# Performance work log

Measured on AMD Instinct MI355X. Metric: run time of the kernel, lower is better.

## Reference

```python
import jax, jax.numpy as jnp
import numpy as np

IN_FEATURES = 16384
OUT_FEATURES = 16384
NNZ = 1_000_000
BATCH = 256


def setup_inputs() -> dict:
    key = jax.random.key(0)
    k1, k2, k3 = jax.random.split(key, 3)
    x = jax.random.normal(k1, (IN_FEATURES, BATCH), dtype=jnp.float32)
    values = jax.random.normal(k2, (NNZ,), dtype=jnp.float32)
    indices = jax.random.randint(k3, (2, NNZ), 0, OUT_FEATURES, dtype=jnp.int64)
    bias = jnp.zeros((OUT_FEATURES, 1), dtype=jnp.float32)
    return {"x": x, "values": values, "indices": indices, "bias": bias}


def reference(x, values, indices, bias):
    # Sparse (COO) matmul: out[r, :] += values[k] * x[c, :] for each nnz (r, c).
    # Equivalent to torch.sparse.mm(W_coo.coalesce(), x) + bias since
    # coalesce() sums duplicate entries and segment_sum does the same.
    row = indices[0]  # [nnz] in [0, OUT_FEATURES)
    col = indices[1]  # [nnz] in [0, IN_FEATURES)
    gathered = values[:, None] * x[col]  # [nnz, B]
    out = jax.ops.segment_sum(gathered, row, num_segments=OUT_FEATURES)  # [out, B]
    return out + bias
```

## Files before the change

### kernel.cpp

```cpp
#include <hip/hip_runtime.h>

typedef unsigned int u32;
typedef unsigned short u16;
typedef unsigned long long u64;

constexpr int OUT_F = 16384;
constexpr int IN_F  = 16384;
constexpr int B_N   = 256;
constexpr int NG    = 512;
constexpr int GCAP  = 2368;
constexpr int BINB  = 4096;


__global__ __launch_bounds__(1024) void prep_k(
    const int* __restrict__ rows, const int* __restrict__ cols,
    const float* __restrict__ vals, const float* __restrict__ x,
    u16* __restrict__ xb, int* __restrict__ gcnt,
    uint2* __restrict__ gbuck, int nnz, int nbin, int n4) {
  const int tid = threadIdx.x;

  if ((int)blockIdx.x >= nbin) {
    const int i2 = blockIdx.x - nbin;
    for (int j = 0; j < 4; ++j) {
      int k4 = i2 * 4096 + j * 1024 + tid;
      if (k4 < n4) {
        float4 v = ((const float4*)x)[k4];
        u32 u0 = __float_as_uint(v.x), u1 = __float_as_uint(v.y),
            u2 = __float_as_uint(v.z), u3 = __float_as_uint(v.w);
        ushort4 r;
        r.x = (u16)((u0 + 0x7FFFu + ((u0 >> 16) & 1u)) >> 16);
        r.y = (u16)((u1 + 0x7FFFu + ((u1 >> 16) & 1u)) >> 16);
        r.z = (u16)((u2 + 0x7FFFu + ((u2 >> 16) & 1u)) >> 16);
        r.w = (u16)((u3 + 0x7FFFu + ((u3 >> 16) & 1u)) >> 16);
        ((ushort4*)xb)[k4] = r;
      }
    }
    return;
  }

  __shared__ int   hist[NG], lofs[NG], cur[NG], gbase[NG];
  __shared__ int   wsum[8];
  __shared__ uint2 stage[BINB];
  __shared__ int   tgt[BINB];

  const int base = blockIdx.x * BINB;
  const int nval = min(BINB, nnz - base);
  if (tid < NG) hist[tid] = 0;
  __syncthreads();

  int r[4]; u32 c[4]; float v[4]; bool ok[4];
#pragma unroll
  for (int i = 0; i < 4; ++i) {
    int k = base + i * 1024 + tid;
    ok[i] = k < nnz;
    if (ok[i]) {
      r[i] = __builtin_nontemporal_load(&rows[k]);
      c[i] = (u32)__builtin_nontemporal_load(&cols[k]);
      v[i] = __builtin_nontemporal_load(&vals[k]);
      atomicAdd(&hist[r[i] >> 5], 1);
    }
  }
  __syncthreads();

  const int lane = tid & 63;
  const int wv   = tid >> 6;
  int hv = 0, incl = 0;
  if (tid < NG) {
    hv = hist[tid];
    incl = hv;
#pragma unroll
    for (int d = 1; d < 64; d <<= 1) {
      int t = __shfl_up(incl, d, 64);
      if (lane >= d) incl += t;
    }
    if (lane == 63) wsum[wv] = incl;
  }
  __syncthreads();
  if (tid == 0) {
    int run = 0;
#pragma unroll
    for (int w = 0; w < NG / 64; ++w) { int t = wsum[w]; wsum[w] = run; run += t; }
  }
  __syncthreads();
  if (tid < NG) {
    int excl = incl - hv + wsum[wv];
    lofs[tid] = excl;
    cur[tid]  = excl;
    gbase[tid] = atomicAdd(&gcnt[tid], hv);
  }
  __syncthreads();

#pragma unroll
  for (int i = 0; i < 4; ++i) {
    if (ok[i]) {
      int g   = r[i] >> 5;
      int pos = atomicAdd(&cur[g], 1);
      stage[pos].x = (c[i] << 5) | (u32)(r[i] & 31);
      stage[pos].y = __float_as_uint(v[i]);
      int w = gbase[g] + (pos - lofs[g]);
      tgt[pos] = (w < GCAP) ? (g * GCAP + w) : -1;
    }
  }
  __syncthreads();

#pragma unroll
  for (int j = 0; j < 4; ++j) {
    int idx = j * 1024 + tid;
    if (idx < nval) {
      int t = tgt[idx];
      if (t >= 0) gbuck[t] = stage[idx];
    }
  }
}

__global__ __launch_bounds__(1024) void sortspmm_k(
    const int* __restrict__ gcnt, const uint2* __restrict__ gbuck,
    const u16* __restrict__ xb, const float* __restrict__ bias,
    float* __restrict__ out) {
  __shared__ int hist[2048];
  __shared__ int wsum[16];
  __shared__ u32 pk_lds[GCAP];
  __shared__ int rs[32], rc[32];
  const int tid = threadIdx.x;
  const int g   = blockIdx.x;
  int cnt = gcnt[g];
  if (cnt > GCAP) cnt = GCAP;
  const uint2* bk = gbuck + (size_t)g * GCAP;

#pragma unroll
  for (int i = 0; i < 2; ++i) hist[i * 1024 + tid] = 0;
  __syncthreads();

  uint2 e[3]; int bin[3]; bool ok[3];
#pragma unroll
  for (int i = 0; i < 3; ++i) {
    int k = i * 1024 + tid;
    ok[i] = k < cnt;
    if (ok[i]) {
      u64 q = __builtin_nontemporal_load((const u64*)&bk[k]);
      e[i].x = (u32)q; e[i].y = (u32)(q >> 32);
      bin[i] = (int)(((e[i].x & 31u) << 6) | (e[i].x >> 13));
      atomicAdd(&hist[bin[i]], 1);
    }
  }
  __syncthreads();

  const int lane = tid & 63;
  const int wv   = tid >> 6;
  int loc0 = hist[tid * 2], loc1 = hist[tid * 2 + 1];
  int s = loc0 + loc1;
  int incl = s;
#pragma unroll
  for (int d = 1; d < 64; d <<= 1) {
    int t = __shfl_up(incl, d, 64);
    if (lane >= d) incl += t;
  }
  if (lane == 63) wsum[wv] = incl;
  __syncthreads();
  if (tid == 0) {
    int run = 0;
#pragma unroll
    for (int w = 0; w < 16; ++w) { int t = wsum[w]; wsum[w] = run; run += t; }
  }
  __syncthreads();
  int excl = incl - s + wsum[wv];
  hist[tid * 2]     = excl;
  hist[tid * 2 + 1] = excl + loc0;
  __syncthreads();

  if (tid < 32) {
    int lo = hist[tid << 6];
    int hi = (tid == 31) ? cnt : hist[(tid + 1) << 6];
    rs[tid] = lo;
    rc[tid] = hi - lo;
  }
  __syncthreads();

#pragma unroll
  for (int i = 0; i < 3; ++i) {
    if (ok[i]) {
      int pos = atomicAdd(&hist[bin[i]], 1);
      u32 col = e[i].x >> 5;
      pk_lds[pos] = (col << 18) | (e[i].y >> 14);
    }
  }
  __syncthreads();

  const int wid = tid >> 6;
  const int r0g = g * 32;

  for (int rr = 0; rr < 2; ++rr) {
    const int fr   = wid * 2 + rr;
    const int st   = rs[fr];
    const int cntr = rc[fr];
    float a0 = 0.f, a1 = 0.f, a2 = 0.f, a3 = 0.f;
    for (int base = 0; base < cntr; base += 64) {
      const int m = min(64, cntr - base);
      u32 pk = 0;
      if (lane < m) pk = pk_lds[st + base + lane];
      int j = 0;
      for (; j + 8 <= m; j += 8) {
        u32 e0 = (u32)__builtin_amdgcn_readlane((int)pk, j);
        u32 e1 = (u32)__builtin_amdgcn_readlane((int)pk, j + 1);
        u32 e2 = (u32)__builtin_amdgcn_readlane((int)pk, j + 2);
        u32 e3 = (u32)__builtin_amdgcn_readlane((int)pk, j + 3);
        u32 e4 = (u32)__builtin_amdgcn_readlane((int)pk, j + 4);
        u32 e5 = (u32)__builtin_amdgcn_readlane((int)pk, j + 5);
        u32 e6 = (u32)__builtin_amdgcn_readlane((int)pk, j + 6);
        u32 e7 = (u32)__builtin_amdgcn_readlane((int)pk, j + 7);
        uint2 x0 = ((const uint2*)(xb + ((size_t)(e0 >> 18) << 8)))[lane];
        uint2 x1 = ((const uint2*)(xb + ((size_t)(e1 >> 18) << 8)))[lane];
        uint2 x2 = ((const uint2*)(xb + ((size_t)(e2 >> 18) << 8)))[lane];
        uint2 x3 = ((const uint2*)(xb + ((size_t)(e3 >> 18) << 8)))[lane];
        uint2 x4 = ((const uint2*)(xb + ((size_t)(e4 >> 18) << 8)))[lane];
        uint2 x5 = ((const uint2*)(xb + ((size_t)(e5 >> 18) << 8)))[lane];
        uint2 x6 = ((const uint2*)(xb + ((size_t)(e6 >> 18) << 8)))[lane];
        uint2 x7 = ((const uint2*)(xb + ((size_t)(e7 >> 18) << 8)))[lane];
        float v0 = __uint_as_float(e0 << 14), v1 = __uint_as_float(e1 << 14);
        float v2 = __uint_as_float(e2 << 14), v3 = __uint_as_float(e3 << 14);
        float v4 = __uint_as_float(e4 << 14), v5 = __uint_as_float(e5 << 14);
        float v6 = __uint_as_float(e6 << 14), v7 = __uint_as_float(e7 << 14);
        a0 = fmaf(v0, __uint_as_float(x0.x << 16), a0);
        a1 = fmaf(v0, __uint_as_float(x0.x & 0xFFFF0000u), a1);
        a2 = fmaf(v0, __uint_as_float(x0.y << 16), a2);
        a3 = fmaf(v0, __uint_as_float(x0.y & 0xFFFF0000u), a3);
        a0 = fmaf(v1, __uint_as_float(x1.x << 16), a0);
        a1 = fmaf(v1, __uint_as_float(x1.x & 0xFFFF0000u), a1);
        a2 = fmaf(v1, __uint_as_float(x1.y << 16), a2);
        a3 = fmaf(v1, __uint_as_float(x1.y & 0xFFFF0000u), a3);
        a0 = fmaf(v2, __uint_as_float(x2.x << 16), a0);
        a1 = fmaf(v2, __uint_as_float(x2.x & 0xFFFF0000u), a1);
        a2 = fmaf(v2, __uint_as_float(x2.y << 16), a2);
        a3 = fmaf(v2, __uint_as_float(x2.y & 0xFFFF0000u), a3);
        a0 = fmaf(v3, __uint_as_float(x3.x << 16), a0);
        a1 = fmaf(v3, __uint_as_float(x3.x & 0xFFFF0000u), a1);
        a2 = fmaf(v3, __uint_as_float(x3.y << 16), a2);
        a3 = fmaf(v3, __uint_as_float(x3.y & 0xFFFF0000u), a3);
        a0 = fmaf(v4, __uint_as_float(x4.x << 16), a0);
        a1 = fmaf(v4, __uint_as_float(x4.x & 0xFFFF0000u), a1);
        a2 = fmaf(v4, __uint_as_float(x4.y << 16), a2);
        a3 = fmaf(v4, __uint_as_float(x4.y & 0xFFFF0000u), a3);
        a0 = fmaf(v5, __uint_as_float(x5.x << 16), a0);
        a1 = fmaf(v5, __uint_as_float(x5.x & 0xFFFF0000u), a1);
        a2 = fmaf(v5, __uint_as_float(x5.y << 16), a2);
        a3 = fmaf(v5, __uint_as_float(x5.y & 0xFFFF0000u), a3);
        a0 = fmaf(v6, __uint_as_float(x6.x << 16), a0);
        a1 = fmaf(v6, __uint_as_float(x6.x & 0xFFFF0000u), a1);
        a2 = fmaf(v6, __uint_as_float(x6.y << 16), a2);
        a3 = fmaf(v6, __uint_as_float(x6.y & 0xFFFF0000u), a3);
        a0 = fmaf(v7, __uint_as_float(x7.x << 16), a0);
        a1 = fmaf(v7, __uint_as_float(x7.x & 0xFFFF0000u), a1);
        a2 = fmaf(v7, __uint_as_float(x7.y << 16), a2);
        a3 = fmaf(v7, __uint_as_float(x7.y & 0xFFFF0000u), a3);
      }
      for (; j < m; ++j) {
        u32 ee = (u32)__builtin_amdgcn_readlane((int)pk, j);
        float v = __uint_as_float(ee << 14);
        uint2 xx = ((const uint2*)(xb + ((size_t)(ee >> 18) << 8)))[lane];
        a0 = fmaf(v, __uint_as_float(xx.x << 16), a0);
        a1 = fmaf(v, __uint_as_float(xx.x & 0xFFFF0000u), a1);
        a2 = fmaf(v, __uint_as_float(xx.y << 16), a2);
        a3 = fmaf(v, __uint_as_float(xx.y & 0xFFFF0000u), a3);
      }
    }
    const int rout = r0g + fr;
    const float bv = bias[rout];
    u64 lo = ((u64)__float_as_uint(a1 + bv) << 32) | (u64)__float_as_uint(a0 + bv);
    u64 hi = ((u64)__float_as_uint(a3 + bv) << 32) | (u64)__float_as_uint(a2 + bv);
    u64* dst = (u64*)(out + (size_t)rout * B_N + lane * 4);
    __builtin_nontemporal_store(lo, dst);
    __builtin_nontemporal_store(hi, dst + 1);
  }
}


__global__ __launch_bounds__(256) void hist_k(const int* __restrict__ rows,
                                              int* __restrict__ counts, int nnz) {
  int k = blockIdx.x * 256 + threadIdx.x;
  if (k < nnz) atomicAdd(&counts[rows[k]], 1);
}

__global__ __launch_bounds__(1024) void scan_k(const int* __restrict__ counts,
                                               int* __restrict__ offsets,
                                               int* __restrict__ cursor) {
  __shared__ int part[1024];
  const int tid  = threadIdx.x;
  const int base = tid * 16;
  int loc[16];
  int s = 0;
#pragma unroll
  for (int i = 0; i < 16; ++i) { loc[i] = counts[base + i]; s += loc[i]; }
  part[tid] = s;
  __syncthreads();
  for (int off = 1; off < 1024; off <<= 1) {
    int v = (tid >= off) ? part[tid - off] : 0;
    __syncthreads();
    part[tid] += v;
    __syncthreads();
  }
  int run = (tid == 0) ? 0 : part[tid - 1];
#pragma unroll
  for (int i = 0; i < 16; ++i) {
    offsets[base + i] = run;
    cursor[base + i]  = run;
    run += loc[i];
  }
  if (tid == 1023) offsets[OUT_F] = run;
}

__global__ __launch_bounds__(256) void scatter_k(const int* __restrict__ rows,
                                                 const int* __restrict__ colsIn,
                                                 const float* __restrict__ vals,
                                                 int* __restrict__ cursor,
                                                 int* __restrict__ colsOut,
                                                 float* __restrict__ valsOut,
                                                 int nnz) {
  int k = blockIdx.x * 256 + threadIdx.x;
  if (k < nnz) {
    int r   = rows[k];
    int pos = atomicAdd(&cursor[r], 1);
    colsOut[pos] = colsIn[k];
    valsOut[pos] = vals[k];
  }
}

__global__ __launch_bounds__(256) void spmm_k(const int* __restrict__ offsets,
                                              const int* __restrict__ cols,
                                              const float* __restrict__ vals,
                                              const float* __restrict__ x,
                                              const float* __restrict__ bias,
                                              float* __restrict__ out) {
  __shared__ int   c_lds[256];
  __shared__ float v_lds[256];
  const int r = blockIdx.x;
  const int b = threadIdx.x;
  const int start = offsets[r];
  const int end   = offsets[r + 1];
  float acc = 0.f;
  for (int basei = start; basei < end; basei += 256) {
    const int n = min(256, end - basei);
    if (threadIdx.x < n) {
      c_lds[threadIdx.x] = cols[basei + threadIdx.x];
      v_lds[threadIdx.x] = vals[basei + threadIdx.x];
    }
    __syncthreads();
    for (int j = 0; j < n; ++j) {
      acc = fmaf(v_lds[j], x[(size_t)c_lds[j] * B_N + b], acc);
    }
    __syncthreads();
  }
  out[(size_t)r * B_N + b] = acc + bias[r];
}


__global__ __launch_bounds__(256) void initout_k(const float* __restrict__ bias,
                                                 float* __restrict__ out) {
  int i = blockIdx.x * 256 + threadIdx.x;
  out[i] = bias[i >> 8];
}

__global__ __launch_bounds__(256) void atomic_k(const int* __restrict__ rows,
                                                const int* __restrict__ colsIn,
                                                const float* __restrict__ vals,
                                                const float* __restrict__ x,
                                                float* __restrict__ out, int nnz) {
  int k = blockIdx.x;
  if (k < nnz) {
    int r = rows[k], c = colsIn[k];
    float v = vals[k];
    int b = threadIdx.x;
    atomicAdd(&out[(size_t)r * B_N + b], v * x[(size_t)c * B_N + b]);
  }
}

extern "C" void kernel_launch(void* const* d_in, const int* in_sizes, int n_in,
                              void* d_out, int out_size, void* d_ws, size_t ws_size,
                              hipStream_t stream) {
  const float* x      = (const float*)d_in[0];
  const float* values = (const float*)d_in[1];
  const int*   idx    = (const int*)d_in[2];
  const float* bias   = (const float*)d_in[3];
  float* out = (float*)d_out;

  const int nnz = in_sizes[2] / 2;
  const int* rows   = idx;
  const int* colsIn = idx + nnz;

  char* ws = (char*)d_ws;
  auto align256 = [](size_t v) { return (v + 255) & ~(size_t)255; };

  size_t t1_gcnt  = 0;
  size_t t1_gbuck = align256(t1_gcnt + (size_t)NG * 4);
  size_t t1_xb    = align256(t1_gbuck + (size_t)NG * GCAP * 8);
  size_t t1_need  = align256(t1_xb + (size_t)IN_F * B_N * 2);

  size_t t2_counts  = 0;
  size_t t2_offsets = align256(t2_counts + (size_t)OUT_F * 4);
  size_t t2_cursor  = align256(t2_offsets + ((size_t)OUT_F + 1) * 4);
  size_t t2_cols    = align256(t2_cursor + (size_t)OUT_F * 4);
  size_t t2_vals    = align256(t2_cols + (size_t)nnz * 4);
  size_t t2_need    = align256(t2_vals + (size_t)nnz * 4);

  if (ws_size >= t1_need) {
    int*   gcnt  = (int*)(ws + t1_gcnt);
    uint2* gbuck = (uint2*)(ws + t1_gbuck);
    u16*   xb    = (u16*)(ws + t1_xb);

    const int n4   = IN_F * B_N / 4;
    const int nbin = (nnz + BINB - 1) / BINB;
    const int nxc  = (n4 + 4095) / 4096;

    hipMemsetAsync(gcnt, 0, (size_t)NG * 4, stream);
    prep_k<<<nbin + nxc, 1024, 0, stream>>>(rows, colsIn, values, x, xb, gcnt,
                                            gbuck, nnz, nbin, n4);
    sortspmm_k<<<NG, 1024, 0, stream>>>(gcnt, gbuck, xb, bias, out);
  } else if (ws_size >= t2_need) {
    int*   counts  = (int*)(ws + t2_counts);
    int*   offsets = (int*)(ws + t2_offsets);
    int*   cursor  = (int*)(ws + t2_cursor);
    int*   colsB   = (int*)(ws + t2_cols);
    float* valsB   = (float*)(ws + t2_vals);

    const int nblk = (nnz + 255) / 256;
    hipMemsetAsync(counts, 0, (size_t)OUT_F * 4, stream);
    hist_k<<<nblk, 256, 0, stream>>>(rows, counts, nnz);
    scan_k<<<1, 1024, 0, stream>>>(counts, offsets, cursor);
    scatter_k<<<nblk, 256, 0, stream>>>(rows, colsIn, values, cursor, colsB, valsB, nnz);
    spmm_k<<<OUT_F, 256, 0, stream>>>(offsets, colsB, valsB, x, bias, out);
  } else {
    initout_k<<<(out_size + 255) / 256, 256, 0, stream>>>(bias, out);
    atomic_k<<<nnz, 256, 0, stream>>>(rows, colsIn, values, x, out, nnz);
  }
}
```

Baseline: 68.24 us.

## Fuse memset, prep and sort-spmm into one cooperative kernel with grid syncs

Replaces the memset plus two kernel launches with a single cooperative kernel of 512 blocks. Each block zeroes its group count, then blocks either bin nonzeros or convert x to bf16, a grid sync follows, and then every block does the per-group sort and gather. The aim is to remove launch gaps and inter-kernel drain between stages, at the cost of grid-wide barriers, 1024-thread blocks that must all be co-resident, and fewer blocks for the x conversion. The old multi-kernel path stays as a fallback if the cooperative launch fails.

```diff
diff --git a/kernel.cpp b/kernel.cpp
--- a/kernel.cpp
+++ b/kernel.cpp
@@ -1,4 +1,5 @@
 #include <hip/hip_runtime.h>
+#include <hip/hip_cooperative_groups.h>
 
 typedef unsigned int u32;
 typedef unsigned short u16;
@@ -11,186 +12,12 @@
 constexpr int GCAP  = 2368;
 constexpr int BINB  = 4096;
 
-
-__global__ __launch_bounds__(1024) void prep_k(
-    const int* __restrict__ rows, const int* __restrict__ cols,
-    const float* __restrict__ vals, const float* __restrict__ x,
-    u16* __restrict__ xb, int* __restrict__ gcnt,
-    uint2* __restrict__ gbuck, int nnz, int nbin, int n4) {
-  const int tid = threadIdx.x;
-
-  if ((int)blockIdx.x >= nbin) {
-    const int i2 = blockIdx.x - nbin;
-    for (int j = 0; j < 4; ++j) {
-      int k4 = i2 * 4096 + j * 1024 + tid;
-      if (k4 < n4) {
-        float4 v = ((const float4*)x)[k4];
-        u32 u0 = __float_as_uint(v.x), u1 = __float_as_uint(v.y),
-            u2 = __float_as_uint(v.z), u3 = __float_as_uint(v.w);
-        ushort4 r;
-        r.x = (u16)((u0 + 0x7FFFu + ((u0 >> 16) & 1u)) >> 16);
-        r.y = (u16)((u1 + 0x7FFFu + ((u1 >> 16) & 1u)) >> 16);
-        r.z = (u16)((u2 + 0x7FFFu + ((u2 >> 16) & 1u)) >> 16);
-        r.w = (u16)((u3 + 0x7FFFu + ((u3 >> 16) & 1u)) >> 16);
-        ((ushort4*)xb)[k4] = r;
-      }
-    }
-    return;
-  }
-
-  __shared__ int   hist[NG], lofs[NG], cur[NG], gbase[NG];
-  __shared__ int   wsum[8];
-  __shared__ uint2 stage[BINB];
-  __shared__ int   tgt[BINB];
-
-  const int base = blockIdx.x * BINB;
-  const int nval = min(BINB, nnz - base);
-  if (tid < NG) hist[tid] = 0;
-  __syncthreads();
-
-  int r[4]; u32 c[4]; float v[4]; bool ok[4];
-#pragma unroll
-  for (int i = 0; i < 4; ++i) {
-    int k = base + i * 1024 + tid;
-    ok[i] = k < nnz;
-    if (ok[i]) {
-      r[i] = __builtin_nontemporal_load(&rows[k]);
-      c[i] = (u32)__builtin_nontemporal_load(&cols[k]);
-      v[i] = __builtin_nontemporal_load(&vals[k]);
-      atomicAdd(&hist[r[i] >> 5], 1);
-    }
-  }
-  __syncthreads();
-
-  const int lane = tid & 63;
-  const int wv   = tid >> 6;
-  int hv = 0, incl = 0;
-  if (tid < NG) {
-    hv = hist[tid];
-    incl = hv;
-#pragma unroll
-    for (int d = 1; d < 64; d <<= 1) {
-      int t = __shfl_up(incl, d, 64);
-      if (lane >= d) incl += t;
-    }
-    if (lane == 63) wsum[wv] = incl;
-  }
-  __syncthreads();
-  if (tid == 0) {
-    int run = 0;
-#pragma unroll
-    for (int w = 0; w < NG / 64; ++w) { int t = wsum[w]; wsum[w] = run; run += t; }
-  }
-  __syncthreads();
-  if (tid < NG) {
-    int excl = incl - hv + wsum[wv];
-    lofs[tid] = excl;
-    cur[tid]  = excl;
-    gbase[tid] = atomicAdd(&gcnt[tid], hv);
-  }
-  __syncthreads();
-
-#pragma unroll
-  for (int i = 0; i < 4; ++i) {
-    if (ok[i]) {
-      int g   = r[i] >> 5;
-      int pos = atomicAdd(&cur[g], 1);
-      stage[pos].x = (c[i] << 5) | (u32)(r[i] & 31);
-      stage[pos].y = __float_as_uint(v[i]);
-      int w = gbase[g] + (pos - lofs[g]);
-      tgt[pos] = (w < GCAP) ? (g * GCAP + w) : -1;
-    }
-  }
-  __syncthreads();
-
-#pragma unroll
-  for (int j = 0; j < 4; ++j) {
-    int idx = j * 1024 + tid;
-    if (idx < nval) {
-      int t = tgt[idx];
-      if (t >= 0) gbuck[t] = stage[idx];
-    }
-  }
-}
-
-__global__ __launch_bounds__(1024) void sortspmm_k(
-    const int* __restrict__ gcnt, const uint2* __restrict__ gbuck,
-    const u16* __restrict__ xb, const float* __restrict__ bias,
-    float* __restrict__ out) {
-  __shared__ int hist[2048];
-  __shared__ int wsum[16];
-  __shared__ u32 pk_lds[GCAP];
-  __shared__ int rs[32], rc[32];
-  const int tid = threadIdx.x;
-  const int g   = blockIdx.x;
-  int cnt = gcnt[g];
-  if (cnt > GCAP) cnt = GCAP;
-  const uint2* bk = gbuck + (size_t)g * GCAP;
-
-#pragma unroll
-  for (int i = 0; i < 2; ++i) hist[i * 1024 + tid] = 0;
-  __syncthreads();
-
-  uint2 e[3]; int bin[3]; bool ok[3];
-#pragma unroll
-  for (int i = 0; i < 3; ++i) {
-    int k = i * 1024 + tid;
-    ok[i] = k < cnt;
-    if (ok[i]) {
-      u64 q = __builtin_nontemporal_load((const u64*)&bk[k]);
-      e[i].x = (u32)q; e[i].y = (u32)(q >> 32);
-      bin[i] = (int)(((e[i].x & 31u) << 6) | (e[i].x >> 13));
-      atomicAdd(&hist[bin[i]], 1);
-    }
-  }
-  __syncthreads();
-
-  const int lane = tid & 63;
-  const int wv   = tid >> 6;
-  int loc0 = hist[tid * 2], loc1 = hist[tid * 2 + 1];
-  int s = loc0 + loc1;
-  int incl = s;
-#pragma unroll
-  for (int d = 1; d < 64; d <<= 1) {
-    int t = __shfl_up(incl, d, 64);
-    if (lane >= d) incl += t;
-  }
-  if (lane == 63) wsum[wv] = incl;
-  __syncthreads();
-  if (tid == 0) {
-    int run = 0;
-#pragma unroll
-    for (int w = 0; w < 16; ++w) { int t = wsum[w]; wsum[w] = run; run += t; }
-  }
-  __syncthreads();
-  int excl = incl - s + wsum[wv];
-  hist[tid * 2]     = excl;
-  hist[tid * 2 + 1] = excl + loc0;
-  __syncthreads();
-
-  if (tid < 32) {
-    int lo = hist[tid << 6];
-    int hi = (tid == 31) ? cnt : hist[(tid + 1) << 6];
-    rs[tid] = lo;
-    rc[tid] = hi - lo;
-  }
-  __syncthreads();
-
-#pragma unroll
-  for (int i = 0; i < 3; ++i) {
-    if (ok[i]) {
-      int pos = atomicAdd(&hist[bin[i]], 1);
-      u32 col = e[i].x >> 5;
-      pk_lds[pos] = (col << 18) | (e[i].y >> 14);
-    }
-  }
-  __syncthreads();
-
-  const int wid = tid >> 6;
+__device__ __forceinline__ void gather_rows(
+    const int* rs, const int* rc, const u32* pk_lds, const u16* xb,
+    const float* bias, float* out, int g, int lane, int wv, int rows_per_wave) {
   const int r0g = g * 32;
-
-  for (int rr = 0; rr < 2; ++rr) {
-    const int fr   = wid * 2 + rr;
+  for (int rr = 0; rr < rows_per_wave; ++rr) {
+    const int fr   = wv * rows_per_wave + rr;
     const int st   = rs[fr];
     const int cntr = rc[fr];
     float a0 = 0.f, a1 = 0.f, a2 = 0.f, a3 = 0.f;
@@ -273,6 +100,360 @@
   }
 }
 
+struct SmemA {
+  int histA[NG]; int lofs[NG]; int cur[NG]; int gbase[NG]; int wsumA[8];
+  uint2 stage[BINB]; int tgt[BINB];
+};
+struct SmemB {
+  int histB[2048]; int wsumB[16]; u32 pk_lds[GCAP]; int rs[32]; int rc[32];
+};
+union SmemU { SmemA a; SmemB b; };
+
+__global__ __launch_bounds__(1024) void mega_k(
+    const int* __restrict__ rows, const int* __restrict__ cols,
+    const float* __restrict__ vals, const float* __restrict__ x,
+    u16* __restrict__ xb, int* __restrict__ gcnt, uint2* __restrict__ gbuck,
+    const float* __restrict__ bias, float* __restrict__ out,
+    int nnz, int nbin, int n4) {
+  __shared__ SmemU sm;
+  cooperative_groups::grid_group grid = cooperative_groups::this_grid();
+  const int tid  = threadIdx.x;
+  const int b    = blockIdx.x;
+  const int lane = tid & 63;
+  const int wv   = tid >> 6;
+
+  if (tid == 0) gcnt[b] = 0;
+  grid.sync();
+
+  if (b < nbin) {
+    const int base = b * BINB;
+    const int nval = min(BINB, nnz - base);
+    if (tid < NG) sm.a.histA[tid] = 0;
+    __syncthreads();
+
+    int r[4]; u32 c[4]; float v[4]; bool ok[4];
+#pragma unroll
+    for (int i = 0; i < 4; ++i) {
+      int k = base + i * 1024 + tid;
+      ok[i] = k < nnz;
+      if (ok[i]) {
+        r[i] = __builtin_nontemporal_load(&rows[k]);
+        c[i] = (u32)__builtin_nontemporal_load(&cols[k]);
+        v[i] = __builtin_nontemporal_load(&vals[k]);
+        atomicAdd(&sm.a.histA[r[i] >> 5], 1);
+      }
+    }
+    __syncthreads();
+
+    int hv = 0, incl = 0;
+    if (tid < NG) {
+      hv = sm.a.histA[tid];
+      incl = hv;
+#pragma unroll
+      for (int d = 1; d < 64; d <<= 1) {
+        int t = __shfl_up(incl, d, 64);
+        if (lane >= d) incl += t;
+      }
+      if (lane == 63) sm.a.wsumA[wv] = incl;
+    }
+    __syncthreads();
+    if (tid == 0) {
+      int run = 0;
+#pragma unroll
+      for (int w = 0; w < NG / 64; ++w) { int t = sm.a.wsumA[w]; sm.a.wsumA[w] = run; run += t; }
+    }
+    __syncthreads();
+    if (tid < NG) {
+      int excl = incl - hv + sm.a.wsumA[wv];
+      sm.a.lofs[tid] = excl;
+      sm.a.cur[tid]  = excl;
+      sm.a.gbase[tid] = atomicAdd(&gcnt[tid], hv);
+    }
+    __syncthreads();
+
+#pragma unroll
+    for (int i = 0; i < 4; ++i) {
+      if (ok[i]) {
+        int g   = r[i] >> 5;
+        int pos = atomicAdd(&sm.a.cur[g], 1);
+        sm.a.stage[pos].x = (c[i] << 5) | (u32)(r[i] & 31);
+        sm.a.stage[pos].y = __float_as_uint(v[i]);
+        int w = sm.a.gbase[g] + (pos - sm.a.lofs[g]);
+        sm.a.tgt[pos] = (w < GCAP) ? (g * GCAP + w) : -1;
+      }
+    }
+    __syncthreads();
+
+#pragma unroll
+    for (int j = 0; j < 4; ++j) {
+      int idx = j * 1024 + tid;
+      if (idx < nval) {
+        int t = sm.a.tgt[idx];
+        if (t >= 0) gbuck[t] = sm.a.stage[idx];
+      }
+    }
+  } else {
+    const int nxc = NG - nbin;
+    const int per = (n4 + nxc - 1) / nxc;
+    const int s0  = (b - nbin) * per;
+    const int cnt4 = min(per, n4 - s0);
+    for (int j = tid; j < cnt4; j += 1024) {
+      float4 v = ((const float4*)x)[s0 + j];
+      u32 u0 = __float_as_uint(v.x), u1 = __float_as_uint(v.y),
+          u2 = __float_as_uint(v.z), u3 = __float_as_uint(v.w);
+      ushort4 rr;
+      rr.x = (u16)((u0 + 0x7FFFu + ((u0 >> 16) & 1u)) >> 16);
+      rr.y = (u16)((u1 + 0x7FFFu + ((u1 >> 16) & 1u)) >> 16);
+      rr.z = (u16)((u2 + 0x7FFFu + ((u2 >> 16) & 1u)) >> 16);
+      rr.w = (u16)((u3 + 0x7FFFu + ((u3 >> 16) & 1u)) >> 16);
+      ((ushort4*)xb)[s0 + j] = rr;
+    }
+  }
+  grid.sync();
+
+  const int g = b;
+  int cnt = gcnt[g];
+  if (cnt > GCAP) cnt = GCAP;
+  const uint2* bk = gbuck + (size_t)g * GCAP;
+
+#pragma unroll
+  for (int i = 0; i < 2; ++i) sm.b.histB[i * 1024 + tid] = 0;
+  __syncthreads();
+
+  uint2 e[3]; int bin[3]; bool ok[3];
+#pragma unroll
+  for (int i = 0; i < 3; ++i) {
+    int k = i * 1024 + tid;
+    ok[i] = k < cnt;
+    if (ok[i]) {
+      u64 q = __builtin_nontemporal_load((const u64*)&bk[k]);
+      e[i].x = (u32)q; e[i].y = (u32)(q >> 32);
+      bin[i] = (int)(((e[i].x & 31u) << 6) | (e[i].x >> 13));
+      atomicAdd(&sm.b.histB[bin[i]], 1);
+    }
+  }
+  __syncthreads();
+
+  int loc0 = sm.b.histB[tid * 2], loc1 = sm.b.histB[tid * 2 + 1];
+  int s = loc0 + loc1;
+  int incl = s;
+#pragma unroll
+  for (int d = 1; d < 64; d <<= 1) {
+    int t = __shfl_up(incl, d, 64);
+    if (lane >= d) incl += t;
+  }
+  if (lane == 63) sm.b.wsumB[wv] = incl;
+  __syncthreads();
+  if (tid == 0) {
+    int run = 0;
+#pragma unroll
+    for (int w = 0; w < 16; ++w) { int t = sm.b.wsumB[w]; sm.b.wsumB[w] = run; run += t; }
+  }
+  __syncthreads();
+  int excl = incl - s + sm.b.wsumB[wv];
+  sm.b.histB[tid * 2]     = excl;
+  sm.b.histB[tid * 2 + 1] = excl + loc0;
+  __syncthreads();
+
+  if (tid < 32) {
+    int lo = sm.b.histB[tid << 6];
+    int hi = (tid == 31) ? cnt : sm.b.histB[(tid + 1) << 6];
+    sm.b.rs[tid] = lo;
+    sm.b.rc[tid] = hi - lo;
+  }
+  __syncthreads();
+
+#pragma unroll
+  for (int i = 0; i < 3; ++i) {
+    if (ok[i]) {
+      int pos = atomicAdd(&sm.b.histB[bin[i]], 1);
+      u32 col = e[i].x >> 5;
+      sm.b.pk_lds[pos] = (col << 18) | (e[i].y >> 14);
+    }
+  }
+  __syncthreads();
+
+  gather_rows(sm.b.rs, sm.b.rc, sm.b.pk_lds, xb, bias, out, g, lane, wv, 2);
+}
+
+
+__global__ __launch_bounds__(1024) void prep_k(
+    const int* __restrict__ rows, const int* __restrict__ cols,
+    const float* __restrict__ vals, const float* __restrict__ x,
+    u16* __restrict__ xb, int* __restrict__ gcnt,
+    uint2* __restrict__ gbuck, int nnz, int nbin, int n4) {
+  const int tid = threadIdx.x;
+
+  if ((int)blockIdx.x >= nbin) {
+    const int i2 = blockIdx.x - nbin;
+    for (int j = 0; j < 4; ++j) {
+      int k4 = i2 * 4096 + j * 1024 + tid;
+      if (k4 < n4) {
+        float4 v = ((const float4*)x)[k4];
+        u32 u0 = __float_as_uint(v.x), u1 = __float_as_uint(v.y),
+            u2 = __float_as_uint(v.z), u3 = __float_as_uint(v.w);
+        ushort4 r;
+        r.x = (u16)((u0 + 0x7FFFu + ((u0 >> 16) & 1u)) >> 16);
+        r.y = (u16)((u1 + 0x7FFFu + ((u1 >> 16) & 1u)) >> 16);
+        r.z = (u16)((u2 + 0x7FFFu + ((u2 >> 16) & 1u)) >> 16);
+        r.w = (u16)((u3 + 0x7FFFu + ((u3 >> 16) & 1u)) >> 16);
+        ((ushort4*)xb)[k4] = r;
+      }
+    }
+    return;
+  }
+
+  __shared__ int   hist[NG], lofs[NG], cur[NG], gbase[NG];
+  __shared__ int   wsum[8];
+  __shared__ uint2 stage[BINB];
+  __shared__ int   tgt[BINB];
+
+  const int base = blockIdx.x * BINB;
+  const int nval = min(BINB, nnz - base);
+  if (tid < NG) hist[tid] = 0;
+  __syncthreads();
+
+  int r[4]; u32 c[4]; float v[4]; bool ok[4];
+#pragma unroll
+  for (int i = 0; i < 4; ++i) {
+    int k = base + i * 1024 + tid;
+    ok[i] = k < nnz;
+    if (ok[i]) {
+      r[i] = __builtin_nontemporal_load(&rows[k]);
+      c[i] = (u32)__builtin_nontemporal_load(&cols[k]);
+      v[i] = __builtin_nontemporal_load(&vals[k]);
+      atomicAdd(&hist[r[i] >> 5], 1);
+    }
+  }
+  __syncthreads();
+
+  const int lane = tid & 63;
+  const int wv   = tid >> 6;
+  int hv = 0, incl = 0;
+  if (tid < NG) {
+    hv = hist[tid];
+    incl = hv;
+#pragma unroll
+    for (int d = 1; d < 64; d <<= 1) {
+      int t = __shfl_up(incl, d, 64);
+      if (lane >= d) incl += t;
+    }
+    if (lane == 63) wsum[wv] = incl;
+  }
+  __syncthreads();
+  if (tid == 0) {
+    int run = 0;
+#pragma unroll
+    for (int w = 0; w < NG / 64; ++w) { int t = wsum[w]; wsum[w] = run; run += t; }
+  }
+  __syncthreads();
+  if (tid < NG) {
+    int excl = incl - hv + wsum[wv];
+    lofs[tid] = excl;
+    cur[tid]  = excl;
+    gbase[tid] = atomicAdd(&gcnt[tid], hv);
+  }
+  __syncthreads();
+
+#pragma unroll
+  for (int i = 0; i < 4; ++i) {
+    if (ok[i]) {
+      int g   = r[i] >> 5;
+      int pos = atomicAdd(&cur[g], 1);
+      stage[pos].x = (c[i] << 5) | (u32)(r[i] & 31);
+      stage[pos].y = __float_as_uint(v[i]);
+      int w = gbase[g] + (pos - lofs[g]);
+      tgt[pos] = (w < GCAP) ? (g * GCAP + w) : -1;
+    }
+  }
+  __syncthreads();
+
+#pragma unroll
+  for (int j = 0; j < 4; ++j) {
+    int idx = j * 1024 + tid;
+    if (idx < nval) {
+      int t = tgt[idx];
+      if (t >= 0) gbuck[t] = stage[idx];
+    }
+  }
+}
+
+__global__ __launch_bounds__(1024) void sortspmm_k(
+    const int* __restrict__ gcnt, const uint2* __restrict__ gbuck,
+    const u16* __restrict__ xb, const float* __restrict__ bias,
+    float* __restrict__ out) {
+  __shared__ int hist[2048];
+  __shared__ int wsum[16];
+  __shared__ u32 pk_lds[GCAP];
+  __shared__ int rs[32], rc[32];
+  const int tid = threadIdx.x;
+  const int g   = blockIdx.x;
+  int cnt = gcnt[g];
+  if (cnt > GCAP) cnt = GCAP;
+  const uint2* bk = gbuck + (size_t)g * GCAP;
+
+#pragma unroll
+  for (int i = 0; i < 2; ++i) hist[i * 1024 + tid] = 0;
+  __syncthreads();
+
+  uint2 e[3]; int bin[3]; bool ok[3];
+#pragma unroll
+  for (int i = 0; i < 3; ++i) {
+    int k = i * 1024 + tid;
+    ok[i] = k < cnt;
+    if (ok[i]) {
+      u64 q = __builtin_nontemporal_load((const u64*)&bk[k]);
+      e[i].x = (u32)q; e[i].y = (u32)(q >> 32);
+      bin[i] = (int)(((e[i].x & 31u) << 6) | (e[i].x >> 13));
+      atomicAdd(&hist[bin[i]], 1);
+    }
+  }
+  __syncthreads();
+
+  const int lane = tid & 63;
+  const int wv   = tid >> 6;
+  int loc0 = hist[tid * 2], loc1 = hist[tid * 2 + 1];
+  int s = loc0 + loc1;
+  int incl = s;
+#pragma unroll
+  for (int d = 1; d < 64; d <<= 1) {
+    int t = __shfl_up(incl, d, 64);
+    if (lane >= d) incl += t;
+  }
+  if (lane == 63) wsum[wv] = incl;
+  __syncthreads();
+  if (tid == 0) {
+    int run = 0;
+#pragma unroll
+    for (int w = 0; w < 16; ++w) { int t = wsum[w]; wsum[w] = run; run += t; }
+  }
+  __syncthreads();
+  int excl = incl - s + wsum[wv];
+  hist[tid * 2]     = excl;
+  hist[tid * 2 + 1] = excl + loc0;
+  __syncthreads();
+
+  if (tid < 32) {
+    int lo = hist[tid << 6];
+    int hi = (tid == 31) ? cnt : hist[(tid + 1) << 6];
+    rs[tid] = lo;
+    rc[tid] = hi - lo;
+  }
+  __syncthreads();
+
+#pragma unroll
+  for (int i = 0; i < 3; ++i) {
+    if (ok[i]) {
+      int pos = atomicAdd(&hist[bin[i]], 1);
+      u32 col = e[i].x >> 5;
+      pk_lds[pos] = (col << 18) | (e[i].y >> 14);
+    }
+  }
+  __syncthreads();
+
+  gather_rows(rs, rc, pk_lds, xb, bias, out, g, lane, wv, 2);
+}
+
 
 __global__ __launch_bounds__(256) void hist_k(const int* __restrict__ rows,
                                               int* __restrict__ counts, int nnz) {
@@ -382,7 +563,7 @@
   const float* bias   = (const float*)d_in[3];
   float* out = (float*)d_out;
 
-  const int nnz = in_sizes[2] / 2;
+  int nnz = in_sizes[2] / 2;
   const int* rows   = idx;
   const int* colsIn = idx + nnz;
 
@@ -401,19 +582,29 @@
   size_t t2_vals    = align256(t2_cols + (size_t)nnz * 4);
   size_t t2_need    = align256(t2_vals + (size_t)nnz * 4);
 
+  int n4   = IN_F * B_N / 4;
+  int nbin = (nnz + BINB - 1) / BINB;
+
   if (ws_size >= t1_need) {
     int*   gcnt  = (int*)(ws + t1_gcnt);
     uint2* gbuck = (uint2*)(ws + t1_gbuck);
     u16*   xb    = (u16*)(ws + t1_xb);
 
-    const int n4   = IN_F * B_N / 4;
-    const int nbin = (nnz + BINB - 1) / BINB;
-    const int nxc  = (n4 + 4095) / 4096;
-
-    hipMemsetAsync(gcnt, 0, (size_t)NG * 4, stream);
-    prep_k<<<nbin + nxc, 1024, 0, stream>>>(rows, colsIn, values, x, xb, gcnt,
-                                            gbuck, nnz, nbin, n4);
-    sortspmm_k<<<NG, 1024, 0, stream>>>(gcnt, gbuck, xb, bias, out);
+    hipError_t err = hipErrorUnknown;
+    if (nbin < NG) {
+      void* args[] = {(void*)&rows, (void*)&colsIn, (void*)&values, (void*)&x,
+                      (void*)&xb,   (void*)&gcnt,   (void*)&gbuck,  (void*)&bias,
+                      (void*)&out,  (void*)&nnz,    (void*)&nbin,   (void*)&n4};
+      err = hipLaunchCooperativeKernel((void*)mega_k, dim3(NG), dim3(1024),
+                                       args, 0, stream);
+    }
+    if (err != hipSuccess) {
+      hipMemsetAsync(gcnt, 0, (size_t)NG * 4, stream);
+      const int nxc = (n4 + 4095) / 4096;
+      prep_k<<<nbin + nxc, 1024, 0, stream>>>(rows, colsIn, values, x, xb, gcnt,
+                                              gbuck, nnz, nbin, n4);
+      sortspmm_k<<<NG, 1024, 0, stream>>>(gcnt, gbuck, xb, bias, out);
+    }
   } else if (ws_size >= t2_need) {
     int*   counts  = (int*)(ws + t2_counts);
     int*   offsets = (int*)(ws + t2_offsets);
```

Measured after the change: 166.5 us. 144% more time.
